# Optimization experiments

Measured on AMD Instinct MI355X. Metric: run time of the kernel, lower is better.

## Reference

```python
import jax, jax.numpy as jnp
import numpy as np

NOISE_LOG_PROP = -2.0  # log prior mass of the noise/outlier component
N_UNITS = 256


def setup_inputs() -> dict:
    key = jax.random.key(0)
    k1, k2, k3, k4, k5 = jax.random.split(key, 5)
    n_spikes, rank, nc = 131072, 8, 16
    K = 10  # n_candidates + n_candidates*n_search + n_explore = 3 + 6 + 1
    return {
        "features": jax.random.normal(k1, (n_spikes, rank, nc), dtype=jnp.float32),
        "means": jax.random.normal(k2, (N_UNITS, rank, nc), dtype=jnp.float32),
        "log_noise_var": jax.random.normal(k3, (rank, nc), dtype=jnp.float32),
        "log_proportions": jax.random.normal(k4, (N_UNITS,), dtype=jnp.float32),
        "candidates": jax.random.randint(k5, (n_spikes, K), 0, N_UNITS, dtype=jnp.int64),
    }


def reference(features, means, log_noise_var, log_proportions, candidates):
    """Truncated E-step batch: gather per-candidate unit params, compute
    Gaussian log-likelihoods + noise component, soft responsibilities, and
    scatter-add per-unit sufficient statistics [weighted feature sums | counts].
    Returns stats of shape (n_units, d+1); last column is N (soft counts),
    mirroring the original's m[:, :, :-1] count-column layout."""
    n, r, c = features.shape
    U = means.shape[0]
    K = candidates.shape[1]
    d = r * c
    x = features.reshape(n, d)                      # [n, d]
    mu = means.reshape(U, d)                        # [U, d]
    inv_var = jnp.exp(-log_noise_var).reshape(d)    # diagonal noise precision
    logdet = jnp.sum(log_noise_var)

    # gather candidate unit means: irregular gather [n, K, d]
    cand_mu = mu[candidates]
    diff = x[:, None, :] - cand_mu
    maha = jnp.einsum("nkd,d,nkd->nk", diff, inv_var, diff)
    ll = -0.5 * (logdet + maha) + log_proportions[candidates]  # [n, K]

    # noise (zero-mean) component log-lik per spike
    noise_maha = jnp.einsum("nd,d,nd->n", x, inv_var, x)
    noise_ll = -0.5 * (logdet + noise_maha) + NOISE_LOG_PROP   # [n]

    logits = jnp.concatenate([ll, noise_ll[:, None]], axis=1)  # [n, K+1]
    resp = jax.nn.softmax(logits, axis=1)

    # sufficient statistics: append ones column so counts N ride along as
    # the last column (matches the original m[..., :-1] convention)
    x_aug = jnp.concatenate([x, jnp.ones((n, 1), x.dtype)], axis=1)  # [n, d+1]
    contrib = (resp[:, :K, None] * x_aug[:, None, :]).reshape(n * K, d + 1)
    stats = jax.ops.segment_sum(contrib, candidates.reshape(-1), num_segments=U)
    return stats
```

## Files before the change

kernel.cpp:

```cpp
#include <hip/hip_runtime.h>


#define UNITS 256
#define D 128
#define KCAND 10
#define NOISE_LOGIT (-2.0f)
#define ST 129
#define LDS_WORDS (UNITS * ST)
#define SCALE 131072.0f
#define INV_SCALE (1.0f / 131072.0f)
#define GSTATS_ELEMS (UNITS * (D + 1))

template <int CTRL>
__device__ __forceinline__ float dpp_add(float v) {
  const int p = __builtin_amdgcn_update_dpp(0, __float_as_int(v), CTRL, 0xF, 0xF, true);
  return v + __int_as_float(p);
}

__global__ void prep_kernel(const float* __restrict__ means,
                            const float* __restrict__ log_noise_var,
                            const float* __restrict__ log_prop,
                            float* __restrict__ w,
                            float* __restrict__ b,
                            unsigned* __restrict__ gstats) {
  const int u = blockIdx.x;
  const int j = threadIdx.x;
  const float iv = __expf(-log_noise_var[j]);
  const float mu = means[u * D + j];
  const float wv = mu * iv;
  w[u * D + j] = wv;
  float q = mu * wv;
#pragma unroll
  for (int off = 32; off; off >>= 1) q += __shfl_xor(q, off);
  __shared__ float red[2];
  if ((j & 63) == 0) red[j >> 6] = q;
  __syncthreads();
  if (j == 0) b[u] = log_prop[u] - 0.5f * (red[0] + red[1]);
  for (int i = u * D + j; i < GSTATS_ELEMS; i += UNITS * D) gstats[i] = 0u;
}

__global__ void __launch_bounds__(1024, 1) fused_kernel(
    const float* __restrict__ x, const int* __restrict__ cand,
    const float* __restrict__ wmat, const float* __restrict__ bvec,
    unsigned* __restrict__ gstats, int n) {
  extern __shared__ unsigned tile[];
  const int tid = threadIdx.x;
  for (int i = tid; i < LDS_WORDS; i += 1024) tile[i] = 0u;
  __syncthreads();

  const int lane = tid & 63;
  const int wid = tid >> 6;
  const int g = lane >> 3;
  const int l = lane & 7;

  const int spb = n >> 8;
  const int wsp = spb >> 4;
  const int base = blockIdx.x * spb + wid * wsp;

  for (int it = 0; it < (wsp >> 3); ++it) {
    const int spike8 = base + it * 8;
    const int spike = spike8 + g;

    const float* xrow = x + (size_t)spike * D;
    float xv[16];
#pragma unroll
    for (int q = 0; q < 4; ++q) {
      const float4 t = *reinterpret_cast<const float4*>(xrow + q * 32 + l * 4);
      xv[4 * q + 0] = t.x; xv[4 * q + 1] = t.y;
      xv[4 * q + 2] = t.z; xv[4 * q + 3] = t.w;
    }

    int uc[KCAND];
#pragma unroll
    for (int k = 0; k < KCAND; ++k) uc[k] = cand[(size_t)spike * KCAND + k];

    float e[KCAND];
#pragma unroll
    for (int k = 0; k < KCAND; ++k) {
      const float* wrow = wmat + (size_t)uc[k] * D;
      float acc = 0.f;
#pragma unroll
      for (int q = 0; q < 4; ++q) {
        const float4 t = *reinterpret_cast<const float4*>(wrow + q * 32 + l * 4);
        acc = fmaf(xv[4 * q + 0], t.x, acc);
        acc = fmaf(xv[4 * q + 1], t.y, acc);
        acc = fmaf(xv[4 * q + 2], t.z, acc);
        acc = fmaf(xv[4 * q + 3], t.w, acc);
      }
      acc = dpp_add<0xB1>(acc);
      acc = dpp_add<0x4E>(acc);
      acc += __shfl_xor(acc, 4);
      e[k] = acc + bvec[uc[k]];
    }

    float m = NOISE_LOGIT;
#pragma unroll
    for (int k = 0; k < KCAND; ++k) m = fmaxf(m, e[k]);
    float ssum = __expf(NOISE_LOGIT - m);
#pragma unroll
    for (int k = 0; k < KCAND; ++k) { e[k] = __expf(e[k] - m); ssum += e[k]; }
    const float rinv = 1.f / ssum;
#pragma unroll
    for (int k = 0; k < KCAND; ++k) e[k] *= rinv;

    {
      float rsel = e[0]; int usel = uc[0];
#pragma unroll
      for (int k = 1; k < 8; ++k) {
        const bool p = (l == k);
        rsel = p ? e[k] : rsel;
        usel = p ? uc[k] : usel;
      }
      atomicAdd(&tile[usel * ST + D], (unsigned)__float2int_rn(rsel * SCALE));
      const float rs2 = (l == 0) ? e[8] : e[9];
      const int us2 = (l == 0) ? uc[8] : uc[9];
      if (l < 2)
        atomicAdd(&tile[us2 * ST + D], (unsigned)__float2int_rn(rs2 * SCALE));
    }

    float xsa[8], xsb[8];
#pragma unroll
    for (int s = 0; s < 8; ++s) {
      const float* xr = x + (size_t)(spike8 + s) * D;
      xsa[s] = xr[lane] * SCALE;
      xsb[s] = xr[lane + 64] * SCALE;
    }

#pragma unroll
    for (int s = 0; s < 8; ++s) {
#pragma unroll
      for (int k = 0; k < KCAND; ++k) {
        const int u = __builtin_amdgcn_readlane(uc[k], s * 8);
        const float r = __int_as_float(
            __builtin_amdgcn_readlane(__float_as_int(e[k]), s * 8));
        unsigned* rowp = &tile[u * ST];
        atomicAdd(rowp + lane, (unsigned)__float2int_rn(r * xsa[s]));
        atomicAdd(rowp + 64 + lane, (unsigned)__float2int_rn(r * xsb[s]));
      }
    }
  }

  __syncthreads();
  for (int i = tid; i < LDS_WORDS; i += 1024)
    atomicAdd(&gstats[i], tile[i]);
}

__global__ void finish_kernel(const unsigned* __restrict__ gstats,
                              float* __restrict__ out) {
  const int i = blockIdx.x * 256 + threadIdx.x;
  if (i < GSTATS_ELEMS) out[i] = (float)(int)gstats[i] * INV_SCALE;
}

extern "C" void kernel_launch(void* const* d_in, const int* in_sizes, int n_in,
                              void* d_out, int out_size, void* d_ws, size_t ws_size,
                              hipStream_t stream) {
  const float* features = (const float*)d_in[0];
  const float* means    = (const float*)d_in[1];
  const float* lnv      = (const float*)d_in[2];
  const float* lprop    = (const float*)d_in[3];
  const int*   cand     = (const int*)d_in[4];
  float* out = (float*)d_out;

  float* w = (float*)d_ws;
  float* b = w + UNITS * D;
  unsigned* gstats = (unsigned*)(b + UNITS);

  const int n = in_sizes[0] / D;

  prep_kernel<<<UNITS, D, 0, stream>>>(means, lnv, lprop, w, b, gstats);

  const int lds_bytes = LDS_WORDS * sizeof(unsigned);
  hipFuncSetAttribute((const void*)fused_kernel,
                      hipFuncAttributeMaxDynamicSharedMemorySize, lds_bytes);
  fused_kernel<<<256, 1024, lds_bytes, stream>>>(features, cand, w, b, gstats, n);

  finish_kernel<<<(GSTATS_ELEMS + 255) / 256, 256, 0, stream>>>(gstats, out);
}
```

Measured before the change: 171.7 us.

## Replace LDS atomic scatter with dense fp16 responsibility matrix and MFMA

Each block now processes its spikes in 128-spike chunks. It writes per-chunk responsibilities into a dense units×spikes fp16 matrix in LDS, with duplicate candidates pre-summed, and writes the features transposed to fp16 with an appended ones row. The per-unit statistics are then accumulated with 16x16x32 f16 MFMA instructions into register accumulators, replacing the per-element LDS integer atomics. This removes the heavy LDS atomic traffic, in exchange for per-chunk LDS zeroing and extra barriers. Rounding x and responsibilities to fp16 reduces accuracy.

```diff
diff --git a/kernel.cpp b/kernel.cpp
--- a/kernel.cpp
+++ b/kernel.cpp
@@ -5,16 +5,28 @@
 #define D 128
 #define KCAND 10
 #define NOISE_LOGIT (-2.0f)
-#define ST 129
-#define LDS_WORDS (UNITS * ST)
 #define SCALE 131072.0f
 #define INV_SCALE (1.0f / 131072.0f)
 #define GSTATS_ELEMS (UNITS * (D + 1))
+
+#define ROWB 256
+#define PT_ROWS 257
+#define PT_BYTES (PT_ROWS * ROWB)
+#define XT_BASE PT_BYTES
+#define XT_ROWS 144
+#define LDS_BYTES (XT_BASE + XT_ROWS * ROWB)
+
+typedef _Float16 f16x8 __attribute__((ext_vector_type(8)));
+typedef float f32x4 __attribute__((ext_vector_type(4)));
 
 template <int CTRL>
 __device__ __forceinline__ float dpp_add(float v) {
   const int p = __builtin_amdgcn_update_dpp(0, __float_as_int(v), CTRL, 0xF, 0xF, true);
   return v + __int_as_float(p);
+}
+
+__device__ __forceinline__ int swz(int row, int byteInRow) {
+  return byteInRow ^ ((row & 7) << 4);
 }
 
 __global__ void prep_kernel(const float* __restrict__ means,
@@ -39,37 +51,54 @@
   for (int i = u * D + j; i < GSTATS_ELEMS; i += UNITS * D) gstats[i] = 0u;
 }
 
-__global__ void __launch_bounds__(1024, 1) fused_kernel(
+__global__ void __launch_bounds__(1024) fused_kernel(
     const float* __restrict__ x, const int* __restrict__ cand,
     const float* __restrict__ wmat, const float* __restrict__ bvec,
     unsigned* __restrict__ gstats, int n) {
-  extern __shared__ unsigned tile[];
+  extern __shared__ char smem[];
   const int tid = threadIdx.x;
-  for (int i = tid; i < LDS_WORDS; i += 1024) tile[i] = 0u;
-  __syncthreads();
-
   const int lane = tid & 63;
   const int wid = tid >> 6;
   const int g = lane >> 3;
   const int l = lane & 7;
 
+  if (tid < 64)
+    ((unsigned*)(smem + XT_BASE + 128 * ROWB))[tid] = 0x3C003C00u;
+  if (tid < 240)
+    ((uint4*)(smem + XT_BASE + 129 * ROWB))[tid] = make_uint4(0, 0, 0, 0);
+
+  f32x4 acc[9];
+#pragma unroll
+  for (int nt = 0; nt < 9; ++nt) acc[nt] = (f32x4){0.f, 0.f, 0.f, 0.f};
+
   const int spb = n >> 8;
-  const int wsp = spb >> 4;
-  const int base = blockIdx.x * spb + wid * wsp;
-
-  for (int it = 0; it < (wsp >> 3); ++it) {
-    const int spike8 = base + it * 8;
-    const int spike = spike8 + g;
+  const int nchunks = spb >> 7;
+  const int blockBase = blockIdx.x * spb;
+
+  for (int t = 0; t < nchunks; ++t) {
+    __syncthreads();
+    {
+      uint4* p = (uint4*)smem;
+#pragma unroll
+      for (int i = 0; i < 5; ++i) {
+        const int idx = tid + i * 1024;
+        if (idx < (PT_BYTES >> 4)) p[idx] = make_uint4(0, 0, 0, 0);
+      }
+    }
+    __syncthreads();
+
+    const int chunkBase = blockBase + (t << 7);
+    const int spike = chunkBase + (wid << 3) + g;
+    const int sl = (wid << 3) + g;
 
     const float* xrow = x + (size_t)spike * D;
     float xv[16];
 #pragma unroll
     for (int q = 0; q < 4; ++q) {
-      const float4 t = *reinterpret_cast<const float4*>(xrow + q * 32 + l * 4);
-      xv[4 * q + 0] = t.x; xv[4 * q + 1] = t.y;
-      xv[4 * q + 2] = t.z; xv[4 * q + 3] = t.w;
-    }
-
+      const float4 tv = *reinterpret_cast<const float4*>(xrow + q * 32 + l * 4);
+      xv[4 * q + 0] = tv.x; xv[4 * q + 1] = tv.y;
+      xv[4 * q + 2] = tv.z; xv[4 * q + 3] = tv.w;
+    }
     int uc[KCAND];
 #pragma unroll
     for (int k = 0; k < KCAND; ++k) uc[k] = cand[(size_t)spike * KCAND + k];
@@ -78,19 +107,19 @@
 #pragma unroll
     for (int k = 0; k < KCAND; ++k) {
       const float* wrow = wmat + (size_t)uc[k] * D;
-      float acc = 0.f;
+      float a = 0.f;
 #pragma unroll
       for (int q = 0; q < 4; ++q) {
-        const float4 t = *reinterpret_cast<const float4*>(wrow + q * 32 + l * 4);
-        acc = fmaf(xv[4 * q + 0], t.x, acc);
-        acc = fmaf(xv[4 * q + 1], t.y, acc);
-        acc = fmaf(xv[4 * q + 2], t.z, acc);
-        acc = fmaf(xv[4 * q + 3], t.w, acc);
-      }
-      acc = dpp_add<0xB1>(acc);
-      acc = dpp_add<0x4E>(acc);
-      acc += __shfl_xor(acc, 4);
-      e[k] = acc + bvec[uc[k]];
+        const float4 tv = *reinterpret_cast<const float4*>(wrow + q * 32 + l * 4);
+        a = fmaf(xv[4 * q + 0], tv.x, a);
+        a = fmaf(xv[4 * q + 1], tv.y, a);
+        a = fmaf(xv[4 * q + 2], tv.z, a);
+        a = fmaf(xv[4 * q + 3], tv.w, a);
+      }
+      a = dpp_add<0xB1>(a);
+      a = dpp_add<0x4E>(a);
+      a += __shfl_xor(a, 4);
+      e[k] = a + bvec[uc[k]];
     }
 
     float m = NOISE_LOGIT;
@@ -104,45 +133,72 @@
     for (int k = 0; k < KCAND; ++k) e[k] *= rinv;
 
     {
-      float rsel = e[0]; int usel = uc[0];
-#pragma unroll
-      for (int k = 1; k < 8; ++k) {
-        const bool p = (l == k);
-        rsel = p ? e[k] : rsel;
-        usel = p ? uc[k] : usel;
-      }
-      atomicAdd(&tile[usel * ST + D], (unsigned)__float2int_rn(rsel * SCALE));
-      const float rs2 = (l == 0) ? e[8] : e[9];
-      const int us2 = (l == 0) ? uc[8] : uc[9];
+      int u0 = uc[0];
+#pragma unroll
+      for (int k = 1; k < 8; ++k) { const bool p = (l == k); u0 = p ? uc[k] : u0; }
+      bool first = true; float rsum = 0.f;
+#pragma unroll
+      for (int j = 0; j < KCAND; ++j) {
+        const bool eq = (uc[j] == u0);
+        first = first && !(eq && (j < l));
+        rsum += (eq && (j >= l)) ? e[j] : 0.f;
+      }
+      const int urow = first ? u0 : 256;
+      *(_Float16*)(smem + urow * ROWB + swz(urow, sl * 2)) = (_Float16)rsum;
+      const int mk = 8 + l;
+      const int u1 = (l == 0) ? uc[8] : uc[9];
+      bool first2 = true; float rsum2 = 0.f;
+#pragma unroll
+      for (int j = 0; j < KCAND; ++j) {
+        const bool eq = (uc[j] == u1);
+        first2 = first2 && !(eq && (j < mk));
+        rsum2 += (eq && (j >= mk)) ? e[j] : 0.f;
+      }
+      const int urow2 = first2 ? u1 : 256;
       if (l < 2)
-        atomicAdd(&tile[us2 * ST + D], (unsigned)__float2int_rn(rs2 * SCALE));
-    }
-
-    float xsa[8], xsb[8];
+        *(_Float16*)(smem + urow2 * ROWB + swz(urow2, sl * 2)) = (_Float16)rsum2;
+    }
+
 #pragma unroll
     for (int s = 0; s < 8; ++s) {
-      const float* xr = x + (size_t)(spike8 + s) * D;
-      xsa[s] = xr[lane] * SCALE;
-      xsb[s] = xr[lane + 64] * SCALE;
-    }
-
-#pragma unroll
-    for (int s = 0; s < 8; ++s) {
-#pragma unroll
-      for (int k = 0; k < KCAND; ++k) {
-        const int u = __builtin_amdgcn_readlane(uc[k], s * 8);
-        const float r = __int_as_float(
-            __builtin_amdgcn_readlane(__float_as_int(e[k]), s * 8));
-        unsigned* rowp = &tile[u * ST];
-        atomicAdd(rowp + lane, (unsigned)__float2int_rn(r * xsa[s]));
-        atomicAdd(rowp + 64 + lane, (unsigned)__float2int_rn(r * xsb[s]));
+      const float* xr = x + (size_t)(chunkBase + (wid << 3) + s) * D;
+      const int sls = (wid << 3) + s;
+      const float xa = xr[lane];
+      const float xb = xr[lane + 64];
+      *(_Float16*)(smem + XT_BASE + lane * ROWB + swz(lane, sls * 2)) = (_Float16)xa;
+      const int d2 = lane + 64;
+      *(_Float16*)(smem + XT_BASE + d2 * ROWB + swz(d2, sls * 2)) = (_Float16)xb;
+    }
+    __syncthreads();
+
+    const int mm = lane & 15;
+    const int kq = lane >> 4;
+#pragma unroll
+    for (int ks = 0; ks < 4; ++ks) {
+      const int kbyte = ks * 64 + kq * 16;
+      const int arow = (wid << 4) + mm;
+      const f16x8 a = *(const f16x8*)(smem + arow * ROWB + swz(arow, kbyte));
+#pragma unroll
+      for (int nt = 0; nt < 9; ++nt) {
+        const int nrow = (nt << 4) + mm;
+        const f16x8 bfr = *(const f16x8*)(smem + XT_BASE + nrow * ROWB + swz(nrow, kbyte));
+        acc[nt] = __builtin_amdgcn_mfma_f32_16x16x32_f16(a, bfr, acc[nt], 0, 0, 0);
       }
     }
   }
 
-  __syncthreads();
-  for (int i = tid; i < LDS_WORDS; i += 1024)
-    atomicAdd(&gstats[i], tile[i]);
+#pragma unroll
+  for (int nt = 0; nt < 9; ++nt) {
+#pragma unroll
+    for (int r = 0; r < 4; ++r) {
+      const int unit = (wid << 4) + ((lane >> 4) << 2) + r;
+      const int dim = (nt << 4) + (lane & 15);
+      if (dim <= D) {
+        const int q = __float2int_rn(acc[nt][r] * SCALE);
+        atomicAdd(&gstats[unit * (D + 1) + dim], (unsigned)q);
+      }
+    }
+  }
 }
 
 __global__ void finish_kernel(const unsigned* __restrict__ gstats,
@@ -169,10 +225,9 @@
 
   prep_kernel<<<UNITS, D, 0, stream>>>(means, lnv, lprop, w, b, gstats);
 
-  const int lds_bytes = LDS_WORDS * sizeof(unsigned);
   hipFuncSetAttribute((const void*)fused_kernel,
-                      hipFuncAttributeMaxDynamicSharedMemorySize, lds_bytes);
-  fused_kernel<<<256, 1024, lds_bytes, stream>>>(features, cand, w, b, gstats, n);
+                      hipFuncAttributeMaxDynamicSharedMemorySize, LDS_BYTES);
+  fused_kernel<<<n / 512, 1024, LDS_BYTES, stream>>>(features, cand, w, b, gstats, n);
 
   finish_kernel<<<(GSTATS_ELEMS + 255) / 256, 256, 0, stream>>>(gstats, out);
 }
```

Result: slower. 198.3 us (+15.5%).

## Pack two fixed-point accumulators per 64-bit LDS atomic with magic-number bias

Applied to the files above, without the earlier changes.

Each LDS scatter-add now packs two biased 32-bit fixed-point partial sums into one 64-bit atomic, halving the number of shared-memory atomics. Float-to-int rounding uses the magic-constant trick, which adds a positive bias so carries never cross into the high half. A per-row counter in the high word of the count cell records how many adds were made, so the bias can be subtracted during the global flush. This cuts atomic instruction count but relies on the bias bookkeeping staying exact and on the low halves never overflowing.

```diff
diff --git a/kernel.cpp b/kernel.cpp
--- a/kernel.cpp
+++ b/kernel.cpp
@@ -5,10 +5,11 @@
 #define D 128
 #define KCAND 10
 #define NOISE_LOGIT (-2.0f)
-#define ST 129
-#define LDS_WORDS (UNITS * ST)
+#define ROWU64 65
+#define LDS_U64 (UNITS * ROWU64)
 #define SCALE 131072.0f
 #define INV_SCALE (1.0f / 131072.0f)
+#define MAGIC 12582912.0f
 #define GSTATS_ELEMS (UNITS * (D + 1))
 
 template <int CTRL>
@@ -43,9 +44,12 @@
     const float* __restrict__ x, const int* __restrict__ cand,
     const float* __restrict__ wmat, const float* __restrict__ bvec,
     unsigned* __restrict__ gstats, int n) {
-  extern __shared__ unsigned tile[];
+  extern __shared__ unsigned long long tile[];
   const int tid = threadIdx.x;
-  for (int i = tid; i < LDS_WORDS; i += 1024) tile[i] = 0u;
+  {
+    uint4* p = (uint4*)tile;
+    for (int i = tid; i < (LDS_U64 >> 1); i += 1024) p[i] = make_uint4(0, 0, 0, 0);
+  }
   __syncthreads();
 
   const int lane = tid & 63;
@@ -111,11 +115,14 @@
         rsel = p ? e[k] : rsel;
         usel = p ? uc[k] : usel;
       }
-      atomicAdd(&tile[usel * ST + D], (unsigned)__float2int_rn(rsel * SCALE));
+      const unsigned lo = __float_as_uint(fmaf(rsel, SCALE, MAGIC)) - 0x4B400000u;
+      atomicAdd(&tile[usel * ROWU64 + 64], (1ull << 32) | (unsigned long long)lo);
       const float rs2 = (l == 0) ? e[8] : e[9];
       const int us2 = (l == 0) ? uc[8] : uc[9];
-      if (l < 2)
-        atomicAdd(&tile[us2 * ST + D], (unsigned)__float2int_rn(rs2 * SCALE));
+      if (l < 2) {
+        const unsigned lo2 = __float_as_uint(fmaf(rs2, SCALE, MAGIC)) - 0x4B400000u;
+        atomicAdd(&tile[us2 * ROWU64 + 64], (1ull << 32) | (unsigned long long)lo2);
+      }
     }
 
     float xsa[8], xsb[8];
@@ -133,16 +140,24 @@
         const int u = __builtin_amdgcn_readlane(uc[k], s * 8);
         const float r = __int_as_float(
             __builtin_amdgcn_readlane(__float_as_int(e[k]), s * 8));
-        unsigned* rowp = &tile[u * ST];
-        atomicAdd(rowp + lane, (unsigned)__float2int_rn(r * xsa[s]));
-        atomicAdd(rowp + 64 + lane, (unsigned)__float2int_rn(r * xsb[s]));
+        const unsigned lo = __float_as_uint(fmaf(r, xsa[s], MAGIC)) + 0xB5000000u;
+        const unsigned hi = __float_as_uint(fmaf(r, xsb[s], MAGIC)) + 0xB5000000u;
+        atomicAdd(&tile[(unsigned)u * ROWU64 + lane],
+                  ((unsigned long long)hi << 32) | (unsigned long long)lo);
       }
     }
   }
 
   __syncthreads();
-  for (int i = tid; i < LDS_WORDS; i += 1024)
-    atomicAdd(&gstats[i], tile[i]);
+  for (int rr = 0; rr < 16; ++rr) {
+    const int u = wid * 16 + rr;
+    const unsigned long long cell = tile[u * ROWU64 + lane];
+    const unsigned long long tail = tile[u * ROWU64 + 64];
+    const unsigned corr = (unsigned)(tail >> 32) << 22;
+    atomicAdd(&gstats[u * (D + 1) + lane], (unsigned)cell - corr);
+    atomicAdd(&gstats[u * (D + 1) + 64 + lane], (unsigned)(cell >> 32) - corr);
+    if (lane == 0) atomicAdd(&gstats[u * (D + 1) + D], (unsigned)tail);
+  }
 }
 
 __global__ void finish_kernel(const unsigned* __restrict__ gstats,
@@ -169,7 +184,7 @@
 
   prep_kernel<<<UNITS, D, 0, stream>>>(means, lnv, lprop, w, b, gstats);
 
-  const int lds_bytes = LDS_WORDS * sizeof(unsigned);
+  const int lds_bytes = LDS_U64 * 8;
   hipFuncSetAttribute((const void*)fused_kernel,
                       hipFuncAttributeMaxDynamicSharedMemorySize, lds_bytes);
   fused_kernel<<<256, 1024, lds_bytes, stream>>>(features, cand, w, b, gstats, n);
```

Result: no change. 173.5 us (+1.1%).
